# Kernel optimization log

Hardware: AMD Instinct MI355X
Metric: run time of the kernel (lower is better)

Reference implementation:

```python
import jax, jax.numpy as jnp
import numpy as np

SCALE = 0.125  # softmax_scale = 1/sqrt(head_dim=64)


def setup_inputs() -> dict:
    key = jax.random.key(0)
    ks = jax.random.split(key, 5)
    B, H, S, D = 1, 8, 256, 64
    shp = (B, H, S, D)
    return {
        "q": jax.random.normal(ks[0], shp, dtype=jnp.float32),
        "k1": jax.random.normal(ks[1], shp, dtype=jnp.float32),
        "k2": jax.random.normal(ks[2], shp, dtype=jnp.float32),
        "v1": jax.random.normal(ks[3], shp, dtype=jnp.float32),
        "v2": jax.random.normal(ks[4], shp, dtype=jnp.float32),
    }


def reference(q, k1, k2, v1, v2):
    # Trittention: 3-way score over all (i, j) key pairs per query q.
    # s[b,h,q,i,j] = sum_d Q[q,d] * K1[i,d] * K2[j,d]  (scaled)
    B, H, S, D = q.shape
    s = jnp.einsum("bhqd,bhid,bhjd->bhqij", q, k1, k2) * SCALE  # [B,H,S,S,S]
    s_flat = s.reshape(B, H, S, S * S).astype(jnp.float32)
    m = jax.nn.logsumexp(s_flat, axis=-1)               # [B,H,S] flash-style stats
    p = jax.nn.softmax(s_flat, axis=-1).reshape(B, H, S, S, S)
    # O = sum_{i,j} P * (V1_i + V2_j)
    o = (jnp.einsum("bhqij,bhid->bhqd", p, v1)
         + jnp.einsum("bhqij,bhjd->bhqd", p, v2)).astype(q.dtype)
    return o, m
```

## Files before the change

### kernel.cpp

```cpp
#include <hip/hip_runtime.h>
#include <hip/hip_bf16.h>

typedef __attribute__((ext_vector_type(8))) short short8;
typedef __attribute__((ext_vector_type(4))) float f32x4;

static constexpr int S_ = 256;
static constexpr int D_ = 64;
static constexpr int QB = 4;
static constexpr float QSCALE = 0.125f * 1.44269504088896340736f;

__device__ __forceinline__ float bf2f(short b) {
    union { unsigned int u; float f; } x;
    x.u = ((unsigned int)(unsigned short)b) << 16;
    return x.f;
}
__device__ __forceinline__ unsigned cvt_pk_bf16(float lo, float hi) {
    unsigned r;
    asm("v_cvt_pk_bf16_f32 %0, %1, %2" : "=v"(r) : "v"(lo), "v"(hi));
    return r;
}

__global__ __launch_bounds__(256, 3) void tritt_fused(
    const float* __restrict__ qg, const float* __restrict__ k1g,
    const float* __restrict__ k2g, const float* __restrict__ v1g,
    const float* __restrict__ v2g, float* __restrict__ outg)
{
    __shared__ unsigned short sK2[S_ * D_];
    __shared__ float sPi[QB][S_];
    __shared__ float sPj[QB][S_];
    __shared__ float sTmp[4][QB * D_];
    __shared__ float sL[QB];

    const int tid = threadIdx.x;
    const int h  = blockIdx.x >> 6;
    const int q0 = (blockIdx.x & 63) * QB;

    const float* K1h = k1g + h * (S_ * D_);
    const float* K2h = k2g + h * (S_ * D_);

    #pragma unroll
    for (int it = 0; it < 16; ++it) {
        const int e4  = tid * 4 + it * 1024;
        const int row = e4 >> 6, d = e4 & 63;
        const int idx = row * 64 + (d ^ ((row & 7) << 3));
        const float4 b = *(const float4*)(K2h + e4);
        uint2 pb; pb.x = cvt_pk_bf16(b.x, b.y); pb.y = cvt_pk_bf16(b.z, b.w);
        *(uint2*)&sK2[idx] = pb;
    }

    const int w   = tid >> 6;
    const int l   = tid & 63;
    const int g   = l >> 4;
    const int sub = l & 15;

    float qs[2][8];
    {
        const float* Qrow = qg + (h * S_ + q0 + w) * D_;
        #pragma unroll
        for (int k = 0; k < 2; ++k) {
            const f32x4 a = *(const f32x4*)(Qrow + k * 32 + g * 8);
            const f32x4 b = *(const f32x4*)(Qrow + k * 32 + g * 8 + 4);
            qs[k][0]=a[0]*QSCALE; qs[k][1]=a[1]*QSCALE; qs[k][2]=a[2]*QSCALE; qs[k][3]=a[3]*QSCALE;
            qs[k][4]=b[0]*QSCALE; qs[k][5]=b[1]*QSCALE; qs[k][6]=b[2]*QSCALE; qs[k][7]=b[3]*QSCALE;
        }
    }
    __syncthreads();

    float pjreg[16];
    #pragma unroll
    for (int a = 0; a < 16; ++a) pjreg[a] = 0.f;

    for (int pass = 0; pass < 8; ++pass) {
        short8 af[2][2];
        #pragma unroll
        for (int t = 0; t < 2; ++t) {
            const int arow = pass * 32 + t * 16 + sub;
            #pragma unroll
            for (int k = 0; k < 2; ++k) {
                const f32x4 a = *(const f32x4*)(K1h + arow * 64 + k * 32 + g * 8);
                const f32x4 b = *(const f32x4*)(K1h + arow * 64 + k * 32 + g * 8 + 4);
                union { unsigned u[4]; short8 s; } pk;
                pk.u[0] = cvt_pk_bf16(a[0] * qs[k][0], a[1] * qs[k][1]);
                pk.u[1] = cvt_pk_bf16(a[2] * qs[k][2], a[3] * qs[k][3]);
                pk.u[2] = cvt_pk_bf16(b[0] * qs[k][4], b[1] * qs[k][5]);
                pk.u[3] = cvt_pk_bf16(b[2] * qs[k][6], b[3] * qs[k][7]);
                af[t][k] = pk.s;
            }
        }

        float pireg[2][4];
        #pragma unroll
        for (int t = 0; t < 2; ++t)
            #pragma unroll
            for (int r = 0; r < 4; ++r) pireg[t][r] = 0.f;

        #pragma unroll
        for (int jc = 0; jc < 4; ++jc) {
            #pragma unroll
            for (int jt = 0; jt < 4; ++jt) {
                const int jrow = jc * 64 + jt * 16 + sub;
                const int jsw  = (jrow & 7) << 3;
                const short8 b0 = *(const short8*)&sK2[jrow * 64 + ((g * 8) ^ jsw)];
                const short8 b1 = *(const short8*)&sK2[jrow * 64 + ((32 + g * 8) ^ jsw)];
                f32x4 acc0 = __builtin_amdgcn_mfma_f32_16x16x32_bf16(af[0][0], b0, (f32x4){0.f,0.f,0.f,0.f}, 0, 0, 0);
                f32x4 acc1 = __builtin_amdgcn_mfma_f32_16x16x32_bf16(af[1][0], b0, (f32x4){0.f,0.f,0.f,0.f}, 0, 0, 0);
                acc0 = __builtin_amdgcn_mfma_f32_16x16x32_bf16(af[0][1], b1, acc0, 0, 0, 0);
                acc1 = __builtin_amdgcn_mfma_f32_16x16x32_bf16(af[1][1], b1, acc1, 0, 0, 0);
                float e0[4], e1[4];
                #pragma unroll
                for (int r = 0; r < 4; ++r) {
                    e0[r] = __builtin_amdgcn_exp2f(acc0[r]);
                    e1[r] = __builtin_amdgcn_exp2f(acc1[r]);
                    pireg[0][r] += e0[r];
                    pireg[1][r] += e1[r];
                }
                const float s0 = (e0[0] + e0[1]) + (e0[2] + e0[3]);
                const float s1 = (e1[0] + e1[1]) + (e1[2] + e1[3]);
                pjreg[jc * 4 + jt] += s0 + s1;
            }
        }

        #pragma unroll
        for (int t = 0; t < 2; ++t)
            #pragma unroll
            for (int r = 0; r < 4; ++r) {
                float v = pireg[t][r];
                v += __shfl_xor(v, 1); v += __shfl_xor(v, 2);
                v += __shfl_xor(v, 4); v += __shfl_xor(v, 8);
                if (sub == 0) sPi[w][pass * 32 + t * 16 + g * 4 + r] = v;
            }
    }

    #pragma unroll
    for (int jj = 0; jj < 16; ++jj) {
        float v = pjreg[jj];
        v += __shfl_xor(v, 16); v += __shfl_xor(v, 32);
        if (l < 16) sPj[w][jj * 16 + l] = v;
    }

    {
        float ls = sPi[w][l] + sPi[w][64 + l] + sPi[w][128 + l] + sPi[w][192 + l];
        ls += __shfl_xor(ls, 1);  ls += __shfl_xor(ls, 2);  ls += __shfl_xor(ls, 4);
        ls += __shfl_xor(ls, 8);  ls += __shfl_xor(ls, 16); ls += __shfl_xor(ls, 32);
        if (l == 0) sL[w] = ls;
    }
    __syncthreads();

    {
        const int d = l;
        const float* V1h = v1g + h * (S_ * D_);
        const float* V2h = v2g + h * (S_ * D_);
        float p0 = 0.f, p1 = 0.f, p2 = 0.f, p3 = 0.f;
        #pragma unroll 4
        for (int rb = 0; rb < 16; ++rb) {
            const int r0 = w * 64 + rb * 4;
            f32x4 pi0 = *(const f32x4*)&sPi[0][r0];
            f32x4 pi1 = *(const f32x4*)&sPi[1][r0];
            f32x4 pi2 = *(const f32x4*)&sPi[2][r0];
            f32x4 pi3 = *(const f32x4*)&sPi[3][r0];
            f32x4 pj0 = *(const f32x4*)&sPj[0][r0];
            f32x4 pj1 = *(const f32x4*)&sPj[1][r0];
            f32x4 pj2 = *(const f32x4*)&sPj[2][r0];
            f32x4 pj3 = *(const f32x4*)&sPj[3][r0];
            #pragma unroll
            for (int e = 0; e < 4; ++e) {
                const float v1 = V1h[(r0 + e) * D_ + d];
                const float v2 = V2h[(r0 + e) * D_ + d];
                p0 += pi0[e] * v1 + pj0[e] * v2;
                p1 += pi1[e] * v1 + pj1[e] * v2;
                p2 += pi2[e] * v1 + pj2[e] * v2;
                p3 += pi3[e] * v1 + pj3[e] * v2;
            }
        }
        sTmp[w][0 * 64 + d] = p0; sTmp[w][1 * 64 + d] = p1;
        sTmp[w][2 * 64 + d] = p2; sTmp[w][3 * 64 + d] = p3;
    }
    __syncthreads();
    {
        const int q = tid >> 6, d = tid & 63;
        const float oo = sTmp[0][q * 64 + d] + sTmp[1][q * 64 + d]
                       + sTmp[2][q * 64 + d] + sTmp[3][q * 64 + d];
        outg[(h * S_ + q0 + q) * D_ + d] = oo / sL[q];
        if (tid < QB)
            outg[8 * S_ * D_ + h * S_ + q0 + tid] = logf(sL[tid]);
    }
}

extern "C" void kernel_launch(void* const* d_in, const int* in_sizes, int n_in,
                              void* d_out, int out_size, void* d_ws, size_t ws_size,
                              hipStream_t stream) {
    const float* q  = (const float*)d_in[0];
    const float* k1 = (const float*)d_in[1];
    const float* k2 = (const float*)d_in[2];
    const float* v1 = (const float*)d_in[3];
    const float* v2 = (const float*)d_in[4];
    float* out = (float*)d_out;
    tritt_fused<<<dim3(8 * (S_ / QB)), dim3(256), 0, stream>>>(q, k1, k2, v1, v2, out);
}
```

Before: 53.26 us.

## Split key2 dimension across two blocks and add a combine kernel

```diff
diff --git a/kernel.cpp b/kernel.cpp
--- a/kernel.cpp
+++ b/kernel.cpp
@@ -7,43 +7,46 @@
 static constexpr int S_ = 256;
 static constexpr int D_ = 64;
 static constexpr int QB = 4;
+static constexpr int JS = 2;
+static constexpr int JH = S_ / JS;
 static constexpr float QSCALE = 0.125f * 1.44269504088896340736f;
-
-__device__ __forceinline__ float bf2f(short b) {
-    union { unsigned int u; float f; } x;
-    x.u = ((unsigned int)(unsigned short)b) << 16;
-    return x.f;
-}
+static constexpr int NBLK = 8 * (S_ / QB) * JS;
+static constexpr int WS_O_CNT = NBLK * QB * D_;
+
 __device__ __forceinline__ unsigned cvt_pk_bf16(float lo, float hi) {
     unsigned r;
     asm("v_cvt_pk_bf16_f32 %0, %1, %2" : "=v"(r) : "v"(lo), "v"(hi));
     return r;
 }
 
-__global__ __launch_bounds__(256, 3) void tritt_fused(
+__global__ __launch_bounds__(256, 2) void tritt_part(
     const float* __restrict__ qg, const float* __restrict__ k1g,
     const float* __restrict__ k2g, const float* __restrict__ v1g,
-    const float* __restrict__ v2g, float* __restrict__ outg)
+    const float* __restrict__ v2g, float* __restrict__ ws)
 {
-    __shared__ unsigned short sK2[S_ * D_];
+    __shared__ unsigned short sK2[JH * D_];
     __shared__ float sPi[QB][S_];
-    __shared__ float sPj[QB][S_];
+    __shared__ float sPj[QB][JH];
     __shared__ float sTmp[4][QB * D_];
     __shared__ float sL[QB];
 
     const int tid = threadIdx.x;
-    const int h  = blockIdx.x >> 6;
-    const int q0 = (blockIdx.x & 63) * QB;
+    const int bid = blockIdx.x;
+    const int js = bid & 1;
+    const int qt = (bid >> 1) & 63;
+    const int h  = bid >> 7;
+    const int j0 = js * JH;
+    const int q0 = qt * QB;
 
     const float* K1h = k1g + h * (S_ * D_);
     const float* K2h = k2g + h * (S_ * D_);
 
     #pragma unroll
-    for (int it = 0; it < 16; ++it) {
-        const int e4  = tid * 4 + it * 1024;
-        const int row = e4 >> 6, d = e4 & 63;
-        const int idx = row * 64 + (d ^ ((row & 7) << 3));
-        const float4 b = *(const float4*)(K2h + e4);
+    for (int it = 0; it < 8; ++it) {
+        const int e4   = tid * 4 + it * 1024;
+        const int lrow = e4 >> 6, d = e4 & 63;
+        const int idx  = lrow * 64 + (d ^ ((lrow & 7) << 3));
+        const float4 b = *(const float4*)(K2h + j0 * 64 + e4);
         uint2 pb; pb.x = cvt_pk_bf16(b.x, b.y); pb.y = cvt_pk_bf16(b.z, b.w);
         *(uint2*)&sK2[idx] = pb;
     }
@@ -66,9 +69,9 @@
     }
     __syncthreads();
 
-    float pjreg[16];
+    float pjreg[8];
     #pragma unroll
-    for (int a = 0; a < 16; ++a) pjreg[a] = 0.f;
+    for (int a = 0; a < 8; ++a) pjreg[a] = 0.f;
 
     for (int pass = 0; pass < 8; ++pass) {
         short8 af[2][2];
@@ -95,7 +98,7 @@
             for (int r = 0; r < 4; ++r) pireg[t][r] = 0.f;
 
         #pragma unroll
-        for (int jc = 0; jc < 4; ++jc) {
+        for (int jc = 0; jc < 2; ++jc) {
             #pragma unroll
             for (int jt = 0; jt < 4; ++jt) {
                 const int jrow = jc * 64 + jt * 16 + sub;
@@ -132,7 +135,7 @@
     }
 
     #pragma unroll
-    for (int jj = 0; jj < 16; ++jj) {
+    for (int jj = 0; jj < 8; ++jj) {
         float v = pjreg[jj];
         v += __shfl_xor(v, 16); v += __shfl_xor(v, 32);
         if (l < 16) sPj[w][jj * 16 + l] = v;
@@ -158,18 +161,25 @@
             f32x4 pi1 = *(const f32x4*)&sPi[1][r0];
             f32x4 pi2 = *(const f32x4*)&sPi[2][r0];
             f32x4 pi3 = *(const f32x4*)&sPi[3][r0];
+            #pragma unroll
+            for (int e = 0; e < 4; ++e) {
+                const float v1 = V1h[(r0 + e) * D_ + d];
+                p0 += pi0[e] * v1; p1 += pi1[e] * v1;
+                p2 += pi2[e] * v1; p3 += pi3[e] * v1;
+            }
+        }
+        #pragma unroll 4
+        for (int rb = 0; rb < 8; ++rb) {
+            const int r0 = w * 32 + rb * 4;
             f32x4 pj0 = *(const f32x4*)&sPj[0][r0];
             f32x4 pj1 = *(const f32x4*)&sPj[1][r0];
             f32x4 pj2 = *(const f32x4*)&sPj[2][r0];
             f32x4 pj3 = *(const f32x4*)&sPj[3][r0];
             #pragma unroll
             for (int e = 0; e < 4; ++e) {
-                const float v1 = V1h[(r0 + e) * D_ + d];
-                const float v2 = V2h[(r0 + e) * D_ + d];
-                p0 += pi0[e] * v1 + pj0[e] * v2;
-                p1 += pi1[e] * v1 + pj1[e] * v2;
-                p2 += pi2[e] * v1 + pj2[e] * v2;
-                p3 += pi3[e] * v1 + pj3[e] * v2;
+                const float v2 = V2h[(j0 + r0 + e) * D_ + d];
+                p0 += pj0[e] * v2; p1 += pj1[e] * v2;
+                p2 += pj2[e] * v2; p3 += pj3[e] * v2;
             }
         }
         sTmp[w][0 * 64 + d] = p0; sTmp[w][1 * 64 + d] = p1;
@@ -180,10 +190,27 @@
         const int q = tid >> 6, d = tid & 63;
         const float oo = sTmp[0][q * 64 + d] + sTmp[1][q * 64 + d]
                        + sTmp[2][q * 64 + d] + sTmp[3][q * 64 + d];
-        outg[(h * S_ + q0 + q) * D_ + d] = oo / sL[q];
-        if (tid < QB)
-            outg[8 * S_ * D_ + h * S_ + q0 + tid] = logf(sL[tid]);
-    }
+        ws[(bid * QB + q) * D_ + d] = oo;
+        if (tid < QB) ws[WS_O_CNT + bid * QB + tid] = sL[tid];
+    }
+}
+
+__global__ __launch_bounds__(256) void tritt_combine(
+    const float* __restrict__ ws, float* __restrict__ outg)
+{
+    const int flat = blockIdx.x * 256 + threadIdx.x;
+    const int d  = flat & 63;
+    const int q  = (flat >> 6) & 3;
+    const int qt = (flat >> 8) & 63;
+    const int h  = flat >> 14;
+    const int bidA = (h * 64 + qt) * 2;
+    const int ia = (bidA) * QB + q;
+    const int ib = (bidA + 1) * QB + q;
+    const float oA = ws[ia * D_ + d], oB = ws[ib * D_ + d];
+    const float lsum = ws[WS_O_CNT + ia] + ws[WS_O_CNT + ib];
+    outg[(h * S_ + qt * QB + q) * D_ + d] = (oA + oB) / lsum;
+    if (d == 0)
+        outg[8 * S_ * D_ + h * S_ + qt * QB + q] = logf(lsum);
 }
 
 extern "C" void kernel_launch(void* const* d_in, const int* in_sizes, int n_in,
@@ -195,5 +222,7 @@
     const float* v1 = (const float*)d_in[3];
     const float* v2 = (const float*)d_in[4];
     float* out = (float*)d_out;
-    tritt_fused<<<dim3(8 * (S_ / QB)), dim3(256), 0, stream>>>(q, k1, k2, v1, v2, out);
-}
+    float* ws  = (float*)d_ws;
+    tritt_part<<<dim3(NBLK), dim3(256), 0, stream>>>(q, k1, k2, v1, v2, ws);
+    tritt_combine<<<dim3((8 * S_ * D_) / 256), dim3(256), 0, stream>>>(ws, out);
+}
```

Measured after the change: 56.73 us. 6.5% more time.

## Split each query's i-range across two waves, halve queries per block

Applied to the files above, without the earlier changes.

```diff
diff --git a/kernel.cpp b/kernel.cpp
--- a/kernel.cpp
+++ b/kernel.cpp
@@ -6,34 +6,27 @@
 
 static constexpr int S_ = 256;
 static constexpr int D_ = 64;
-static constexpr int QB = 4;
 static constexpr float QSCALE = 0.125f * 1.44269504088896340736f;
 
-__device__ __forceinline__ float bf2f(short b) {
-    union { unsigned int u; float f; } x;
-    x.u = ((unsigned int)(unsigned short)b) << 16;
-    return x.f;
-}
 __device__ __forceinline__ unsigned cvt_pk_bf16(float lo, float hi) {
     unsigned r;
     asm("v_cvt_pk_bf16_f32 %0, %1, %2" : "=v"(r) : "v"(lo), "v"(hi));
     return r;
 }
 
-__global__ __launch_bounds__(256, 3) void tritt_fused(
+__global__ __launch_bounds__(256, 2) void tritt_fused(
     const float* __restrict__ qg, const float* __restrict__ k1g,
     const float* __restrict__ k2g, const float* __restrict__ v1g,
     const float* __restrict__ v2g, float* __restrict__ outg)
 {
     __shared__ unsigned short sK2[S_ * D_];
-    __shared__ float sPi[QB][S_];
-    __shared__ float sPj[QB][S_];
-    __shared__ float sTmp[4][QB * D_];
-    __shared__ float sL[QB];
+    __shared__ float sPi[2][S_];
+    __shared__ float sPjH[4][S_];
 
     const int tid = threadIdx.x;
-    const int h  = blockIdx.x >> 6;
-    const int q0 = (blockIdx.x & 63) * QB;
+    const int qt = blockIdx.x & 127;
+    const int h  = blockIdx.x >> 7;
+    const int q0 = qt * 2;
 
     const float* K1h = k1g + h * (S_ * D_);
     const float* K2h = k2g + h * (S_ * D_);
@@ -48,14 +41,17 @@
         *(uint2*)&sK2[idx] = pb;
     }
 
-    const int w   = tid >> 6;
-    const int l   = tid & 63;
-    const int g   = l >> 4;
-    const int sub = l & 15;
+    const int w     = tid >> 6;
+    const int l     = tid & 63;
+    const int g     = l >> 4;
+    const int sub   = l & 15;
+    const int q     = w & 1;
+    const int ihalf = w >> 1;
+    const int ibase0 = ihalf * 128;
 
     float qs[2][8];
     {
-        const float* Qrow = qg + (h * S_ + q0 + w) * D_;
+        const float* Qrow = qg + (h * S_ + q0 + q) * D_;
         #pragma unroll
         for (int k = 0; k < 2; ++k) {
             const f32x4 a = *(const f32x4*)(Qrow + k * 32 + g * 8);
@@ -70,11 +66,11 @@
     #pragma unroll
     for (int a = 0; a < 16; ++a) pjreg[a] = 0.f;
 
-    for (int pass = 0; pass < 8; ++pass) {
+    for (int pass = 0; pass < 4; ++pass) {
         short8 af[2][2];
         #pragma unroll
         for (int t = 0; t < 2; ++t) {
-            const int arow = pass * 32 + t * 16 + sub;
+            const int arow = ibase0 + pass * 32 + t * 16 + sub;
             #pragma unroll
             for (int k = 0; k < 2; ++k) {
                 const f32x4 a = *(const f32x4*)(K1h + arow * 64 + k * 32 + g * 8);
@@ -127,7 +123,7 @@
                 float v = pireg[t][r];
                 v += __shfl_xor(v, 1); v += __shfl_xor(v, 2);
                 v += __shfl_xor(v, 4); v += __shfl_xor(v, 8);
-                if (sub == 0) sPi[w][pass * 32 + t * 16 + g * 4 + r] = v;
+                if (sub == 0) sPi[q][ibase0 + pass * 32 + t * 16 + g * 4 + r] = v;
             }
     }
 
@@ -135,54 +131,47 @@
     for (int jj = 0; jj < 16; ++jj) {
         float v = pjreg[jj];
         v += __shfl_xor(v, 16); v += __shfl_xor(v, 32);
-        if (l < 16) sPj[w][jj * 16 + l] = v;
-    }
-
-    {
-        float ls = sPi[w][l] + sPi[w][64 + l] + sPi[w][128 + l] + sPi[w][192 + l];
-        ls += __shfl_xor(ls, 1);  ls += __shfl_xor(ls, 2);  ls += __shfl_xor(ls, 4);
-        ls += __shfl_xor(ls, 8);  ls += __shfl_xor(ls, 16); ls += __shfl_xor(ls, 32);
-        if (l == 0) sL[w] = ls;
+        if (l < 16) sPjH[w][jj * 16 + l] = v;
     }
     __syncthreads();
 
+    float* sTmp = (float*)sK2;
     {
         const int d = l;
         const float* V1h = v1g + h * (S_ * D_);
         const float* V2h = v2g + h * (S_ * D_);
-        float p0 = 0.f, p1 = 0.f, p2 = 0.f, p3 = 0.f;
+        float p0 = 0.f, p1 = 0.f;
         #pragma unroll 4
         for (int rb = 0; rb < 16; ++rb) {
             const int r0 = w * 64 + rb * 4;
-            f32x4 pi0 = *(const f32x4*)&sPi[0][r0];
-            f32x4 pi1 = *(const f32x4*)&sPi[1][r0];
-            f32x4 pi2 = *(const f32x4*)&sPi[2][r0];
-            f32x4 pi3 = *(const f32x4*)&sPi[3][r0];
-            f32x4 pj0 = *(const f32x4*)&sPj[0][r0];
-            f32x4 pj1 = *(const f32x4*)&sPj[1][r0];
-            f32x4 pj2 = *(const f32x4*)&sPj[2][r0];
-            f32x4 pj3 = *(const f32x4*)&sPj[3][r0];
+            const f32x4 pi0 = *(const f32x4*)&sPi[0][r0];
+            const f32x4 pi1 = *(const f32x4*)&sPi[1][r0];
+            const f32x4 pa0 = *(const f32x4*)&sPjH[0][r0];
+            const f32x4 pa1 = *(const f32x4*)&sPjH[1][r0];
+            const f32x4 pa2 = *(const f32x4*)&sPjH[2][r0];
+            const f32x4 pa3 = *(const f32x4*)&sPjH[3][r0];
             #pragma unroll
             for (int e = 0; e < 4; ++e) {
                 const float v1 = V1h[(r0 + e) * D_ + d];
                 const float v2 = V2h[(r0 + e) * D_ + d];
-                p0 += pi0[e] * v1 + pj0[e] * v2;
-                p1 += pi1[e] * v1 + pj1[e] * v2;
-                p2 += pi2[e] * v1 + pj2[e] * v2;
-                p3 += pi3[e] * v1 + pj3[e] * v2;
+                p0 += pi0[e] * v1 + (pa0[e] + pa2[e]) * v2;
+                p1 += pi1[e] * v1 + (pa1[e] + pa3[e]) * v2;
             }
         }
-        sTmp[w][0 * 64 + d] = p0; sTmp[w][1 * 64 + d] = p1;
-        sTmp[w][2 * 64 + d] = p2; sTmp[w][3 * 64 + d] = p3;
+        sTmp[w * 128 + 0 * 64 + d] = p0;
+        sTmp[w * 128 + 1 * 64 + d] = p1;
     }
     __syncthreads();
-    {
-        const int q = tid >> 6, d = tid & 63;
-        const float oo = sTmp[0][q * 64 + d] + sTmp[1][q * 64 + d]
-                       + sTmp[2][q * 64 + d] + sTmp[3][q * 64 + d];
-        outg[(h * S_ + q0 + q) * D_ + d] = oo / sL[q];
-        if (tid < QB)
-            outg[8 * S_ * D_ + h * S_ + q0 + tid] = logf(sL[tid]);
+    if (tid < 128) {
+        const int qq = tid >> 6, d = tid & 63;
+        const float oo = sTmp[0 * 128 + qq * 64 + d] + sTmp[1 * 128 + qq * 64 + d]
+                       + sTmp[2 * 128 + qq * 64 + d] + sTmp[3 * 128 + qq * 64 + d];
+        float ls = sPi[qq][d] + sPi[qq][64 + d] + sPi[qq][128 + d] + sPi[qq][192 + d];
+        ls += __shfl_xor(ls, 1);  ls += __shfl_xor(ls, 2);  ls += __shfl_xor(ls, 4);
+        ls += __shfl_xor(ls, 8);  ls += __shfl_xor(ls, 16); ls += __shfl_xor(ls, 32);
+        outg[(h * S_ + q0 + qq) * D_ + d] = oo / ls;
+        if (d == 0)
+            outg[8 * S_ * D_ + h * S_ + q0 + qq] = logf(ls);
     }
 }
 
@@ -195,5 +184,5 @@
     const float* v1 = (const float*)d_in[3];
     const float* v2 = (const float*)d_in[4];
     float* out = (float*)d_out;
-    tritt_fused<<<dim3(8 * (S_ / QB)), dim3(256), 0, stream>>>(q, k1, k2, v1, v2, out);
+    tritt_fused<<<dim3(8 * (S_ / 2)), dim3(256), 0, stream>>>(q, k1, k2, v1, v2, out);
 }
```

Result: faster. 49.22 us (-7.6%).
